# Performance work log

Hardware: AMD Instinct MI355X
Metric: run time of the kernel (lower is better)

## Reference

```python
import jax, jax.numpy as jnp
import numpy as np

CORE_DIM = 128
MEMORY_SLOTS = 64
B, S = 4, 4096


def setup_inputs() -> dict:
    key = jax.random.key(0)
    k1, k2, k3, k4, k5 = jax.random.split(key, 5)
    x = jax.random.normal(k1, (B, S, CORE_DIM), dtype=jnp.float32)
    memory_keys = jax.random.normal(k2, (MEMORY_SLOTS, CORE_DIM), dtype=jnp.float32)
    memory_ops = jax.random.normal(k3, (MEMORY_SLOTS, CORE_DIM, CORE_DIM), dtype=jnp.float32)
    # nn.Linear(core_dim, core_dim): weight [out, in], bias [out]
    bound = 1.0 / np.sqrt(CORE_DIM)
    Wq = jax.random.uniform(k4, (CORE_DIM, CORE_DIM), minval=-bound, maxval=bound, dtype=jnp.float32)
    bq = jax.random.uniform(k5, (CORE_DIM,), minval=-bound, maxval=bound, dtype=jnp.float32)
    return {"input_tensor": x, "memory_keys": memory_keys, "memory_ops": memory_ops, "Wq": Wq, "bq": bq}


def reference(input_tensor, memory_keys, memory_ops, Wq, bq):
    dim = input_tensor.shape[-1]
    # query projection: x @ Wq^T + bq
    queries = jnp.einsum('bsd,ed->bse', input_tensor, Wq) + bq
    # soft attention over memory slots
    attn_logits = jnp.einsum('bsd,md->bsm', queries, memory_keys)
    attn_weights = jax.nn.softmax(attn_logits / jnp.sqrt(jnp.float32(dim)), axis=-1)
    # fused: (sum_m attn[bsm] * ops[m]) @ x[bs]  == sum_m attn[bsm] * (ops[m] @ x[bs])
    processed = jnp.einsum('bsm,mde,bse->bsd', attn_weights, memory_ops, input_tensor)
    return processed
```

## Files before the change

### kernel.cpp

```cpp
#include <hip/hip_runtime.h>

typedef __bf16 bf16x8 __attribute__((ext_vector_type(8)));
typedef float f32x4 __attribute__((ext_vector_type(4)));
typedef unsigned int uint4v __attribute__((ext_vector_type(4)));
typedef unsigned short ushort_t;
typedef unsigned int uint_t;

#define RS 0.08838834764831845f

__device__ __forceinline__ ushort_t f2bf(float f) {
    uint_t u = __float_as_uint(f);
    u += 0x7FFFu + ((u >> 16) & 1u);
    return (ushort_t)(u >> 16);
}
__device__ __forceinline__ uint_t pack2(float a, float b) {
    return (uint_t)f2bf(a) | ((uint_t)f2bf(b) << 16);
}
union U4B8 { uint4v u; bf16x8 b; };
__device__ __forceinline__ bf16x8 as_bf(uint4v u) { U4B8 x; x.u = u; return x.b; }

__device__ __forceinline__ int xfrag(int f, int lane) {
    return f * 1072 + ((lane >> 4) * 272) + ((lane & 15) * 16);
}

__device__ __forceinline__ void gload16(const void* g, void* l) {
    __builtin_amdgcn_global_load_lds(
        (const __attribute__((address_space(1))) void*)g,
        (__attribute__((address_space(3))) void*)l, 16, 0, 0);
}

__global__ __launch_bounds__(256) void prep_kernel(
    const float* __restrict__ ops, const float* __restrict__ keys,
    const float* __restrict__ Wq, const float* __restrict__ bq,
    uint4v* __restrict__ ops_sw, ushort_t* __restrict__ kp_sw,
    float* __restrict__ cb)
{
    const int tid = threadIdx.x;
    const int b = blockIdx.x;
    if (b >= 64) {
        int g = (b - 64) * 256 + tid;
        int L = g & 63, dt = (g >> 6) & 7, ks = (g >> 9) & 3, m = g >> 11;
        int d = dt * 16 + (L & 15);
        int e0 = ks * 32 + ((L >> 4) << 3);
        const float4* s = (const float4*)(ops + (((size_t)(m * 128 + d)) << 7) + e0);
        float4 v0 = s[0], v1 = s[1];
        uint4v o = { pack2(v0.x, v0.y), pack2(v0.z, v0.w),
                     pack2(v1.x, v1.y), pack2(v1.z, v1.w) };
        int h = m * 2048 + (dt >> 2) * 1024 + ks * 256 + (dt & 3) * 64 + L;
        ops_sw[h] = o;
    } else {
        __shared__ float red[256];
        const int m = b;
        const int d = tid & 127, eh = tid >> 7;
        const float* kr = keys + m * 128 + eh * 64;
        const float* wc = Wq + (size_t)(eh * 64) * 128 + d;
        float acc = 0.f;
        #pragma unroll 8
        for (int e = 0; e < 64; ++e)
            acc = fmaf(kr[e], wc[(size_t)e * 128], acc);
        red[tid] = acc;
        __syncthreads();
        if (tid < 128) {
            float v = red[tid] + red[tid + 128];
            int ki = d >> 5, qq = (d >> 3) & 3, j = d & 7;
            kp_sw[((((ki * 4 + (m >> 4)) * 64) + (qq * 16 + (m & 15))) << 3) | j] = f2bf(v);
        } else if (tid >= 192) {
            int lane = tid - 192;
            float p = keys[m * 128 + lane] * bq[lane]
                    + keys[m * 128 + 64 + lane] * bq[64 + lane];
            #pragma unroll
            for (int off = 1; off < 64; off <<= 1) p += __shfl_xor(p, off);
            if (lane == 0) cb[m] = p;
        }
    }
}

__global__ __launch_bounds__(512, 2) void main_kernel(
    const float* __restrict__ x, const float* __restrict__ cb,
    const ushort_t* __restrict__ kp_sw, const uint4v* __restrict__ ops_sw,
    float* __restrict__ out)
{
    __shared__ __align__(16) unsigned char lds[131072];
    uint4v* bb = (uint4v*)lds;
    unsigned char* xs = lds + 32768;
    float* attn_f = (float*)(lds + 98304);

    const int tid = threadIdx.x;
    const int lane = tid & 63;
    const int w = tid >> 6;
    const int q = lane >> 4;
    const int l15 = lane & 15;
    const int tb = blockIdx.x >> 1;
    const int dh = blockIdx.x & 1;
    const int t0 = tb * 128;
    const int slh = w & 1;
    const int dtp = w >> 1;

    auto stage = [&](int pair, int b) {
        uint4v* dst = bb + b * 2048 + w * 64;
        const uint4v* src = ops_sw + (size_t)pair * 4096 + dh * 1024 + w * 64 + lane;
        #pragma unroll
        for (int j = 0; j < 4; ++j) {
            const uint4v* g = src + (j >> 1) * 2048 + (j & 1) * 512;
            gload16((const void*)g, (void*)(dst + j * 512));
        }
    };

    {
        const float4* x4 = (const float4*)(x + (size_t)t0 * 128);
        #pragma unroll
        for (int it = 0; it < 4; ++it) {
            int i = it * 512 + tid;
            int t = i >> 4, kc = i & 15;
            float4 a = x4[t * 32 + kc * 2];
            float4 b2 = x4[t * 32 + kc * 2 + 1];
            uint4v o = { pack2(a.x, a.y), pack2(a.z, a.w),
                         pack2(b2.x, b2.y), pack2(b2.z, b2.w) };
            *(uint4v*)(xs + ((t >> 4) * 4 + (kc >> 2)) * 1072
                          + (kc & 3) * 272 + (t & 15) * 16) = o;
        }
    }
    __syncthreads();

    stage(0, 0);

    {
        f32x4 L0 = {0,0,0,0}, L1 = {0,0,0,0}, L2 = {0,0,0,0}, L3 = {0,0,0,0};
        const uint4v* kpf = (const uint4v*)kp_sw;
        #pragma unroll
        for (int ki = 0; ki < 4; ++ki) {
            bf16x8 a = *(const bf16x8*)(xs + xfrag(w * 4 + ki, lane));
            L0 = __builtin_amdgcn_mfma_f32_16x16x32_bf16(a, as_bf(kpf[(ki*4+0)*64 + lane]), L0, 0,0,0);
            L1 = __builtin_amdgcn_mfma_f32_16x16x32_bf16(a, as_bf(kpf[(ki*4+1)*64 + lane]), L1, 0,0,0);
            L2 = __builtin_amdgcn_mfma_f32_16x16x32_bf16(a, as_bf(kpf[(ki*4+2)*64 + lane]), L2, 0,0,0);
            L3 = __builtin_amdgcn_mfma_f32_16x16x32_bf16(a, as_bf(kpf[(ki*4+3)*64 + lane]), L3, 0,0,0);
        }
        float c0 = cb[l15], c1 = cb[16 + l15], c2 = cb[32 + l15], c3 = cb[48 + l15];
        #pragma unroll
        for (int r = 0; r < 4; ++r) {
            float v0 = (L0[r] + c0) * RS;
            float v1 = (L1[r] + c1) * RS;
            float v2 = (L2[r] + c2) * RS;
            float v3 = (L3[r] + c3) * RS;
            float mx = fmaxf(fmaxf(v0, v1), fmaxf(v2, v3));
            #pragma unroll
            for (int off = 1; off < 16; off <<= 1) mx = fmaxf(mx, __shfl_xor(mx, off));
            float e0 = __expf(v0 - mx), e1 = __expf(v1 - mx),
                  e2 = __expf(v2 - mx), e3 = __expf(v3 - mx);
            float sm = e0 + e1 + e2 + e3;
            #pragma unroll
            for (int off = 1; off < 16; off <<= 1) sm += __shfl_xor(sm, off);
            float inv = 1.0f / sm;
            int t = w * 16 + q * 4 + r;
            int ts = t ^ ((l15 & 7) << 2);
            attn_f[(     l15) * 128 + ts] = e0 * inv;
            attn_f[(16 + l15) * 128 + ts] = e1 * inv;
            attn_f[(32 + l15) * 128 + ts] = e2 * inv;
            attn_f[(48 + l15) * 128 + ts] = e3 * inv;
        }
    }

    bf16x8 A[8][4];
    #pragma unroll
    for (int tf = 0; tf < 8; ++tf)
        #pragma unroll
        for (int ki = 0; ki < 4; ++ki)
            A[tf][ki] = *(const bf16x8*)(xs + xfrag(tf * 4 + ki, lane));

    __syncthreads();

    f32x4 C[8] = {};

    auto computePair = [&](int p) {
        const uint4v* bbuf = bb + (p % 3) * 2048 + slh * 1024 + dtp * 64 + lane;
        const int m = 2 * p + slh;
        const int msw = (m & 7) << 2;
        bf16x8 Bf[4];
        #pragma unroll
        for (int ki = 0; ki < 4; ++ki) Bf[ki] = as_bf(bbuf[ki * 256]);
        #pragma unroll
        for (int th = 0; th < 2; ++th) {
            f32x4 S[4] = {};
            __builtin_amdgcn_s_setprio(1);
            #pragma unroll
            for (int ki = 0; ki < 4; ++ki)
                #pragma unroll
                for (int tf = 0; tf < 4; ++tf)
                    S[tf] = __builtin_amdgcn_mfma_f32_16x16x32_bf16(
                        A[th * 4 + tf][ki], Bf[ki], S[tf], 0, 0, 0);
            __builtin_amdgcn_s_setprio(0);
            #pragma unroll
            for (int tf = 0; tf < 4; ++tf) {
                int ta = ((th * 4 + tf) * 16 + q * 4) ^ msw;
                f32x4 af = *(const f32x4*)&attn_f[m * 128 + ta];
                #pragma unroll
                for (int r = 0; r < 4; ++r)
                    C[th * 4 + tf][r] = fmaf(af[r], S[tf][r], C[th * 4 + tf][r]);
            }
        }
    };

    for (int p = 0; p < 31; ++p) {
        stage(p + 1, (p + 1) % 3);
        asm volatile("s_waitcnt vmcnt(4)" ::: "memory");
        __builtin_amdgcn_s_barrier();
        computePair(p);
    }
    asm volatile("s_waitcnt vmcnt(0)" ::: "memory");
    __builtin_amdgcn_s_barrier();
    computePair(31);

    __syncthreads();
    f32x4* rb = (f32x4*)(lds + 98304);
    if (slh == 1) {
        #pragma unroll
        for (int tf = 0; tf < 8; ++tf)
            rb[dtp * 512 + tf * 64 + lane] = C[tf];
    }
    __syncthreads();
    if (slh == 0) {
        float* op = out + (size_t)t0 * 128 + dh * 64 + dtp * 16 + l15;
        #pragma unroll
        for (int tf = 0; tf < 8; ++tf) {
            f32x4 other = rb[dtp * 512 + tf * 64 + lane];
            #pragma unroll
            for (int r = 0; r < 4; ++r)
                op[(size_t)(tf * 16 + q * 4 + r) * 128] = C[tf][r] + other[r];
        }
    }
}

extern "C" void kernel_launch(void* const* d_in, const int* in_sizes, int n_in,
                              void* d_out, int out_size, void* d_ws, size_t ws_size,
                              hipStream_t stream)
{
    const float* x    = (const float*)d_in[0];
    const float* keys = (const float*)d_in[1];
    const float* ops  = (const float*)d_in[2];
    const float* Wq   = (const float*)d_in[3];
    const float* bq   = (const float*)d_in[4];
    float* out = (float*)d_out;

    char* ws = (char*)d_ws;
    uint4v*   ops_sw = (uint4v*)ws;
    ushort_t* kp_sw  = (ushort_t*)(ws + 2097152);
    float*    cb     = (float*)(ws + 2097152 + 16384);

    prep_kernel<<<576, 256, 0, stream>>>(ops, keys, Wq, bq, ops_sw, kp_sw, cb);
    main_kernel<<<256, 512, 0, stream>>>(x, cb, kp_sw, ops_sw, out);
}
```

Baseline: 108.2 us.

## Make ops staging per-wave private and remove per-iteration block barriers

Each wave now loads into its own LDS region exactly the B fragments it later reads. This removes the block-wide s_barrier that every pair iteration needed. The pipeline is restructured to issue two stages ahead (prefetch depth 3), refill a slot right after its fragments are read into registers, and use vmcnt-based waits only. The xs region is moved to make room, and the loop is unrolled by 3. The risks are LDS region overlap from the new xs offset and the correctness of the vmcnt counts, since waves now rely only on their own loads completing.

```diff
diff --git a/kernel.cpp b/kernel.cpp
--- a/kernel.cpp
+++ b/kernel.cpp
@@ -82,7 +82,7 @@
 {
     __shared__ __align__(16) unsigned char lds[131072];
     uint4v* bb = (uint4v*)lds;
-    unsigned char* xs = lds + 32768;
+    unsigned char* xs = lds + 64000;
     float* attn_f = (float*)(lds + 98304);
 
     const int tid = threadIdx.x;
@@ -96,14 +96,14 @@
     const int slh = w & 1;
     const int dtp = w >> 1;
 
-    auto stage = [&](int pair, int b) {
-        uint4v* dst = bb + b * 2048 + w * 64;
-        const uint4v* src = ops_sw + (size_t)pair * 4096 + dh * 1024 + w * 64 + lane;
-        #pragma unroll
-        for (int j = 0; j < 4; ++j) {
-            const uint4v* g = src + (j >> 1) * 2048 + (j & 1) * 512;
-            gload16((const void*)g, (void*)(dst + j * 512));
-        }
+    auto stage = [&](int pair, int s) {
+        const int m = pair * 2 + slh;
+        uint4v* dst = bb + s * 2048 + w * 256;
+        const uint4v* src = ops_sw + (size_t)m * 2048 + dh * 1024
+                          + dtp * 64 + lane;
+        #pragma unroll
+        for (int ks = 0; ks < 4; ++ks)
+            gload16((const void*)(src + ks * 256), (void*)(dst + ks * 64));
     };
 
     {
@@ -169,15 +169,21 @@
 
     __syncthreads();
 
+    stage(1, 1);
+    stage(2, 2);
+
     f32x4 C[8] = {};
 
-    auto computePair = [&](int p) {
-        const uint4v* bbuf = bb + (p % 3) * 2048 + slh * 1024 + dtp * 64 + lane;
+    auto computeSlot = [&](int p, int s, bool doStage) {
         const int m = 2 * p + slh;
         const int msw = (m & 7) << 2;
         bf16x8 Bf[4];
         #pragma unroll
-        for (int ki = 0; ki < 4; ++ki) Bf[ki] = as_bf(bbuf[ki * 256]);
+        for (int ki = 0; ki < 4; ++ki)
+            Bf[ki] = as_bf(bb[s * 2048 + w * 256 + ki * 64 + lane]);
+        asm volatile("s_waitcnt lgkmcnt(0)" ::: "memory");
+        __builtin_amdgcn_sched_barrier(0);
+        if (doStage) stage(p + 3, s);
         #pragma unroll
         for (int th = 0; th < 2; ++th) {
             f32x4 S[4] = {};
@@ -200,15 +206,15 @@
         }
     };
 
-    for (int p = 0; p < 31; ++p) {
-        stage(p + 1, (p + 1) % 3);
-        asm volatile("s_waitcnt vmcnt(4)" ::: "memory");
-        __builtin_amdgcn_s_barrier();
-        computePair(p);
-    }
+    #pragma unroll 3
+    for (int p = 0; p < 30; ++p) {
+        asm volatile("s_waitcnt vmcnt(8)" ::: "memory");
+        computeSlot(p, p % 3, p < 29);
+    }
+    asm volatile("s_waitcnt vmcnt(4)" ::: "memory");
+    computeSlot(30, 0, false);
     asm volatile("s_waitcnt vmcnt(0)" ::: "memory");
-    __builtin_amdgcn_s_barrier();
-    computePair(31);
+    computeSlot(31, 1, false);
 
     __syncthreads();
     f32x4* rb = (f32x4*)(lds + 98304);
```

After: 183.8 us. 69.9% more time.

## Load memory op fragments directly into registers instead of LDS staging

Applied to the files above, without the earlier changes.

Replaces the triple-buffered global-to-LDS staging of memory_ops fragments, which needed barriers every pair, with direct per-wave global loads into two register buffers that are double-buffered across the pair loop. This removes the per-iteration block barrier and LDS traffic, and shrinks the LDS footprint, which may allow more blocks per CU. In exchange, each wave issues its own global loads, relying on L2 reuse across waves and blocks, and latency hiding now depends on the register prefetch distance and on occupancy.

```diff
diff --git a/kernel.cpp b/kernel.cpp
--- a/kernel.cpp
+++ b/kernel.cpp
@@ -21,12 +21,6 @@
 
 __device__ __forceinline__ int xfrag(int f, int lane) {
     return f * 1072 + ((lane >> 4) * 272) + ((lane & 15) * 16);
-}
-
-__device__ __forceinline__ void gload16(const void* g, void* l) {
-    __builtin_amdgcn_global_load_lds(
-        (const __attribute__((address_space(1))) void*)g,
-        (__attribute__((address_space(3))) void*)l, 16, 0, 0);
 }
 
 __global__ __launch_bounds__(256) void prep_kernel(
@@ -80,10 +74,9 @@
     const ushort_t* __restrict__ kp_sw, const uint4v* __restrict__ ops_sw,
     float* __restrict__ out)
 {
-    __shared__ __align__(16) unsigned char lds[131072];
-    uint4v* bb = (uint4v*)lds;
+    __shared__ __align__(16) unsigned char lds[67072];
+    float* attn_f = (float*)lds;
     unsigned char* xs = lds + 32768;
-    float* attn_f = (float*)(lds + 98304);
 
     const int tid = threadIdx.x;
     const int lane = tid & 63;
@@ -96,16 +89,6 @@
     const int slh = w & 1;
     const int dtp = w >> 1;
 
-    auto stage = [&](int pair, int b) {
-        uint4v* dst = bb + b * 2048 + w * 64;
-        const uint4v* src = ops_sw + (size_t)pair * 4096 + dh * 1024 + w * 64 + lane;
-        #pragma unroll
-        for (int j = 0; j < 4; ++j) {
-            const uint4v* g = src + (j >> 1) * 2048 + (j & 1) * 512;
-            gload16((const void*)g, (void*)(dst + j * 512));
-        }
-    };
-
     {
         const float4* x4 = (const float4*)(x + (size_t)t0 * 128);
         #pragma unroll
@@ -122,8 +105,6 @@
     }
     __syncthreads();
 
-    stage(0, 0);
-
     {
         f32x4 L0 = {0,0,0,0}, L1 = {0,0,0,0}, L2 = {0,0,0,0}, L3 = {0,0,0,0};
         const uint4v* kpf = (const uint4v*)kp_sw;
@@ -169,15 +150,23 @@
 
     __syncthreads();
 
+    const uint4v* myB = ops_sw + (size_t)slh * 2048 + dh * 1024 + dtp * 64 + lane;
+
+    uint4v B0[4], B1[4];
+    auto issue = [&](int p, uint4v (&B)[4]) {
+        const uint4v* src = myB + (size_t)p * 4096;
+        #pragma unroll
+        for (int ks = 0; ks < 4; ++ks) B[ks] = src[ks * 256];
+    };
+
     f32x4 C[8] = {};
 
-    auto computePair = [&](int p) {
-        const uint4v* bbuf = bb + (p % 3) * 2048 + slh * 1024 + dtp * 64 + lane;
+    auto computePair = [&](int p, uint4v (&Bv)[4]) {
         const int m = 2 * p + slh;
         const int msw = (m & 7) << 2;
         bf16x8 Bf[4];
         #pragma unroll
-        for (int ki = 0; ki < 4; ++ki) Bf[ki] = as_bf(bbuf[ki * 256]);
+        for (int ki = 0; ki < 4; ++ki) Bf[ki] = as_bf(Bv[ki]);
         #pragma unroll
         for (int th = 0; th < 2; ++th) {
             f32x4 S[4] = {};
@@ -200,18 +189,20 @@
         }
     };
 
-    for (int p = 0; p < 31; ++p) {
-        stage(p + 1, (p + 1) % 3);
-        asm volatile("s_waitcnt vmcnt(4)" ::: "memory");
-        __builtin_amdgcn_s_barrier();
-        computePair(p);
-    }
-    asm volatile("s_waitcnt vmcnt(0)" ::: "memory");
-    __builtin_amdgcn_s_barrier();
-    computePair(31);
-
-    __syncthreads();
-    f32x4* rb = (f32x4*)(lds + 98304);
+    issue(0, B0);
+    issue(1, B1);
+    #pragma unroll 1
+    for (int p = 0; p < 30; p += 2) {
+        computePair(p, B0);
+        issue(p + 2, B0);
+        computePair(p + 1, B1);
+        issue(p + 3, B1);
+    }
+    computePair(30, B0);
+    computePair(31, B1);
+
+    __syncthreads();
+    f32x4* rb = (f32x4*)lds;
     if (slh == 1) {
         #pragma unroll
         for (int tf = 0; tf < 8; ++tf)
```

Result: slower. 178.5 us (+65.1%).
